# Optimization experiments

Hardware: AMD Instinct MI355X
Metric: run time of the kernel (lower is better)

The kernel has to match this reference:

```python
import jax, jax.numpy as jnp
import numpy as np

A = 16      # attention_beam_width
O = 8       # output_beam_width
H = 1024    # hidden_width
IO = 32     # io_width
DEPTH = 5   # GRU depth
T = 2048    # timesteps


def setup_inputs() -> dict:
    key = jax.random.key(0)
    ks = jax.random.split(key, 6)
    s = lambda k, shape: jax.random.normal(k, shape, dtype=jnp.float32) * 0.02
    return {
        "x": jax.random.normal(ks[0], (T, IO), dtype=jnp.float32),
        "w1": s(ks[1], (H, IO * A)),
        "b1": jnp.zeros((H,), jnp.float32),
        "gru_wih": s(ks[2], (DEPTH, 3 * H, H)),
        "gru_whh": s(ks[3], (DEPTH, 3 * H, H)),
        "gru_bih": jnp.zeros((DEPTH, 3 * H), jnp.float32),
        "gru_bhh": jnp.zeros((DEPTH, 3 * H), jnp.float32),
        "w2": s(ks[4], (IO * O, H)),
        "b2": jnp.zeros((IO * O,), jnp.float32),
    }


def _build_lines(x):
    # create_line at step t = concat([x[t], x[t-2], x[t-3], ..., x[t-A]])
    # (true_history[-i] for i=2..A before x[t] is appended; zeros for t-i < 0)
    Tn = x.shape[0]
    padded = jnp.concatenate([jnp.zeros((A, IO), x.dtype), x], axis=0)
    feats = [x] + [padded[A - i: A - i + Tn] for i in range(2, A + 1)]
    return jnp.concatenate(feats, axis=1)  # [T, IO*A]


def _gru_cell(h, xt, wih, whh, bih, bhh):
    # torch nn.GRU cell math (gate order r, z, n)
    gi = xt @ wih.T + bih      # [3H]
    gh = h @ whh.T + bhh       # [3H]
    i_r, i_z, i_n = jnp.split(gi, 3)
    h_r, h_z, h_n = jnp.split(gh, 3)
    r = jax.nn.sigmoid(i_r + h_r)
    z = jax.nn.sigmoid(i_z + h_z)
    n = jnp.tanh(i_n + r * h_n)
    return (1.0 - z) * n + z * h


def reference(x, w1, b1, gru_wih, gru_whh, gru_bih, gru_bhh, w2, b2):
    Tn = x.shape[0]
    lines = _build_lines(x)          # [T, IO*A]
    pre = lines @ w1.T + b1          # lin1, vectorized over time: [T, H]

    def step(h_all, xt):
        inp = xt
        new_h = []
        for l in range(DEPTH):  # fixed small depth loop
            h_new = _gru_cell(h_all[l], inp, gru_wih[l], gru_whh[l],
                              gru_bih[l], gru_bhh[l])
            new_h.append(h_new)
            inp = h_new
        return jnp.stack(new_h), inp

    h0 = jnp.zeros((DEPTH, H), x.dtype)
    _, gru_outs = jax.lax.scan(step, h0, pre)   # [T, H]
    out = gru_outs @ w2.T + b2                   # lin2: [T, IO*O]
    # per-step output is viewed (O, 1, IO) and cat along dim 1 -> [O, T, IO]
    return out.reshape(Tn, O, IO).transpose(1, 0, 2)
```

## Files before the change

kernel.cpp:

```cpp
#include <hip/hip_runtime.h>
#include <hip/hip_fp16.h>

typedef unsigned int u32;

#define TSTEPS 2048
#define HID    1024
#define NDEPTH 5
#define GSTAGE 51
#define NBLOCKS (NDEPTH * GSTAGE)
#define HCAN   0x7c00u
#define DCAN   0x7c007c00u

typedef _Float16 f16x2v __attribute__((ext_vector_type(2)));

#if defined(__has_builtin)
# if __has_builtin(__builtin_amdgcn_fdot2)
#  define HAVE_FDOT2 1
# endif
#endif

__device__ __forceinline__ float fdot2f(u32 a, u32 b, float c) {
  f16x2v x, y;
  __builtin_memcpy(&x, &a, 4);
  __builtin_memcpy(&y, &b, 4);
#ifdef HAVE_FDOT2
  return __builtin_amdgcn_fdot2(x, y, c, false);
#else
  return c + (float)x[0] * (float)y[0] + (float)x[1] * (float)y[1];
#endif
}

__device__ __forceinline__ u32 pkh(float a, float b) {
  __half2 h = __floats2half2_rn(a, b);
  u32 r;
  __builtin_memcpy(&r, &h, 4);
  return r;
}

__device__ __forceinline__ float dpp_red32(float v) {
  int t, vi;
  __builtin_memcpy(&vi, &v, 4);
  float tf;
#define STEP(CTRL)                                                        \
  t = __builtin_amdgcn_update_dpp(0, vi, CTRL, 0xF, 0xF, true);           \
  __builtin_memcpy(&tf, &t, 4);                                           \
  v += tf;                                                                \
  __builtin_memcpy(&vi, &v, 4);
  STEP(0x111)
  STEP(0x112)
  STEP(0x114)
  STEP(0x118)
  STEP(0x142)
#undef STEP
  return v;
}

__device__ __forceinline__ uint2 spin_load8(const void* p) {
  uint2 v;
  for (;;) {
    asm volatile("global_load_dwordx2 %0, %1, off sc0 sc1\n\ts_waitcnt vmcnt(0)"
                 : "=v"(v) : "v"(p));
    if (((v.x & 0xffffu) != HCAN) & ((v.x >> 16) != HCAN) &
        ((v.y & 0xffffu) != HCAN) & ((v.y >> 16) != HCAN))
      break;
    __builtin_amdgcn_s_sleep(1);
  }
  return v;
}

__global__ __launch_bounds__(256) void fill_canary(u32* __restrict__ p, long n) {
  long i = ((long)blockIdx.x * 256 + threadIdx.x) * 4;
  const long stride = (long)gridDim.x * 256 * 4;
  uint4 c;
  c.x = DCAN; c.y = DCAN; c.z = DCAN; c.w = DCAN;
  for (; i < n; i += stride) *(uint4*)(p + i) = c;
}

__global__ __launch_bounds__(256) void lin1_kernel(
    const float* __restrict__ x, const float* __restrict__ w1,
    const float* __restrict__ b1, __half* __restrict__ X0) {
  __shared__ float lt[32][65];
  __shared__ float wt[128][65];
  const int tid = threadIdx.x;
  const int t0 = blockIdx.x * 32;
  const int h0 = blockIdx.y * 128;
  const int tt0 = (tid & 7) * 4;
  const int hh0 = (tid >> 3) * 4;
  float acc[4][4] = {};
  for (int kc = 0; kc < 512; kc += 64) {
    __syncthreads();
#pragma unroll
    for (int m = 0; m < 8; ++m) {
      int e = tid + m * 256;
      int tt = e >> 6, kk = e & 63;
      int k = kc + kk;
      int a = k >> 5, io = k & 31;
      int d = (a == 0) ? 0 : (a + 1);
      int st = t0 + tt - d;
      lt[tt][kk] = (st >= 0) ? x[st * 32 + io] : 0.f;
    }
#pragma unroll
    for (int m = 0; m < 32; ++m) {
      int e = tid + m * 256;
      int hh = e >> 6, kk = e & 63;
      wt[hh][kk] = w1[(size_t)(h0 + hh) * 512 + kc + kk];
    }
    __syncthreads();
    for (int kk = 0; kk < 64; ++kk) {
      float la[4], wa[4];
#pragma unroll
      for (int i = 0; i < 4; ++i) la[i] = lt[tt0 + i][kk];
#pragma unroll
      for (int j = 0; j < 4; ++j) wa[j] = wt[hh0 + j][kk];
#pragma unroll
      for (int i = 0; i < 4; ++i)
#pragma unroll
        for (int j = 0; j < 4; ++j) acc[i][j] = fmaf(la[i], wa[j], acc[i][j]);
    }
  }
#pragma unroll
  for (int i = 0; i < 4; ++i)
#pragma unroll
    for (int j = 0; j < 4; ++j)
      X0[(size_t)(t0 + tt0 + i) * HID + h0 + hh0 + j] =
          __float2half_rn(acc[i][j] + b1[h0 + hh0 + j]);
}

__global__ __launch_bounds__(512, 2) void gru_pipe(
    const float* __restrict__ wih, const float* __restrict__ whh,
    const float* __restrict__ bih, const float* __restrict__ bhh,
    __half* __restrict__ Xh) {
  const int bid = blockIdx.x;
  const int l   = bid / GSTAGE;
  const int bs  = bid % GSTAGE;
  const int tid = (int)threadIdx.x;
  const int lane = tid & 63;
  const int wv   = tid >> 6;
  const int half = lane >> 5;
  const int kc   = lane & 31;
  const int RG   = 2 * wv + half;

  const int h_base = (bs * HID) / GSTAGE;
  const int h_cnt  = ((bs + 1) * HID) / GSTAGE - h_base;
  const int ndot = 3 * h_cnt;

  const size_t lw = (size_t)l * 3 * HID * HID;
  u32 wA[4][16], wB[4][16];
#pragma unroll
  for (int r = 0; r < 4; ++r) {
    const int d = 4 * RG + r;
    if (d < ndot) {
      const int jj = d / 3, g = d % 3;
      const float* rowA = wih + lw + (size_t)(g * HID + h_base + jj) * HID;
      const float* rowB = whh + lw + (size_t)(g * HID + h_base + jj) * HID;
#pragma unroll
      for (int s = 0; s < 4; ++s) {
        const float4* sa = (const float4*)(rowA + kc * 8 + s * 256);
        const float4* sb = (const float4*)(rowB + kc * 8 + s * 256);
        float4 a0 = sa[0], a1 = sa[1], b0 = sb[0], b1v = sb[1];
        wA[r][s * 4 + 0] = pkh(a0.x, a0.y);
        wA[r][s * 4 + 1] = pkh(a0.z, a0.w);
        wA[r][s * 4 + 2] = pkh(a1.x, a1.y);
        wA[r][s * 4 + 3] = pkh(a1.z, a1.w);
        wB[r][s * 4 + 0] = pkh(b0.x, b0.y);
        wB[r][s * 4 + 1] = pkh(b0.z, b0.w);
        wB[r][s * 4 + 2] = pkh(b1v.x, b1v.y);
        wB[r][s * 4 + 3] = pkh(b1v.z, b1v.w);
      }
    } else {
#pragma unroll
      for (int i = 0; i < 16; ++i) { wA[r][i] = 0u; wB[r][i] = 0u; }
    }
  }

  float b6[6] = {0.f, 0.f, 0.f, 0.f, 0.f, 0.f};
  if (wv == 0 && lane < h_cnt) {
#pragma unroll
    for (int g = 0; g < 3; ++g) {
      b6[g]     = bih[(size_t)l * 3 * HID + g * HID + h_base + lane];
      b6[3 + g] = bhh[(size_t)l * 3 * HID + g * HID + h_base + lane];
    }
  }

  __shared__ __align__(16) __half xbuf[2][HID];
  __shared__ __align__(16) __half hbuf[2][HID];
  __shared__ __align__(16) float scr[2][128];

  const __half* in = Xh + (size_t)l * TSTEPS * HID;
  __half* out      = Xh + (size_t)(l + 1) * TSTEPS * HID;

  if (wv >= 4) {
    const int i = tid - 256;
    uint2 v;
    if (l == 0) v = *(const uint2*)(in + 4 * i);
    else        v = spin_load8(in + 4 * i);
    ((uint2*)xbuf[0])[i] = v;
  }
  float hprev = 0.f;
  __syncthreads();

  for (int t = 0; t < TSTEPS; ++t) {
    const int p = t & 1;

    {
      const uint4* cp = (const uint4*)xbuf[p];
      float a0 = 0.f, a1 = 0.f, a2 = 0.f, a3 = 0.f;
#pragma unroll
      for (int s = 0; s < 4; ++s) {
        uint4 c = cp[kc + 32 * s];
        a0 = fdot2f(wA[0][4 * s + 0], c.x, a0);
        a1 = fdot2f(wA[1][4 * s + 0], c.x, a1);
        a2 = fdot2f(wA[2][4 * s + 0], c.x, a2);
        a3 = fdot2f(wA[3][4 * s + 0], c.x, a3);
        a0 = fdot2f(wA[0][4 * s + 1], c.y, a0);
        a1 = fdot2f(wA[1][4 * s + 1], c.y, a1);
        a2 = fdot2f(wA[2][4 * s + 1], c.y, a2);
        a3 = fdot2f(wA[3][4 * s + 1], c.y, a3);
        a0 = fdot2f(wA[0][4 * s + 2], c.z, a0);
        a1 = fdot2f(wA[1][4 * s + 2], c.z, a1);
        a2 = fdot2f(wA[2][4 * s + 2], c.z, a2);
        a3 = fdot2f(wA[3][4 * s + 2], c.z, a3);
        a0 = fdot2f(wA[0][4 * s + 3], c.w, a0);
        a1 = fdot2f(wA[1][4 * s + 3], c.w, a1);
        a2 = fdot2f(wA[2][4 * s + 3], c.w, a2);
        a3 = fdot2f(wA[3][4 * s + 3], c.w, a3);
      }
      a0 = dpp_red32(a0);
      a1 = dpp_red32(a1);
      a2 = dpp_red32(a2);
      a3 = dpp_red32(a3);
      if ((lane & 31) == 31) {
        float4 s4; s4.x = a0; s4.y = a1; s4.z = a2; s4.w = a3;
        *((float4*)&scr[p][4 * RG]) = s4;
      }
    }

    if (wv < 4) {
      if (t > 0) {
        uint2 v = spin_load8(out + (size_t)(t - 1) * HID + 4 * tid);
        ((uint2*)hbuf[p])[tid] = v;
      } else {
        uint2 z; z.x = 0u; z.y = 0u;
        ((uint2*)hbuf[p])[tid] = z;
      }
    } else {
      const int i = tid - 256;
      const int tn = (t + 1 < TSTEPS) ? (t + 1) : (TSTEPS - 1);
      uint2 v;
      if (l == 0) v = *(const uint2*)(in + (size_t)tn * HID + 4 * i);
      else        v = spin_load8(in + (size_t)tn * HID + 4 * i);
      ((uint2*)xbuf[p ^ 1])[i] = v;
    }
    __syncthreads();

    {
      const uint4* cp = (const uint4*)hbuf[p];
      float a0 = 0.f, a1 = 0.f, a2 = 0.f, a3 = 0.f;
#pragma unroll
      for (int s = 0; s < 4; ++s) {
        uint4 c = cp[kc + 32 * s];
        a0 = fdot2f(wB[0][4 * s + 0], c.x, a0);
        a1 = fdot2f(wB[1][4 * s + 0], c.x, a1);
        a2 = fdot2f(wB[2][4 * s + 0], c.x, a2);
        a3 = fdot2f(wB[3][4 * s + 0], c.x, a3);
        a0 = fdot2f(wB[0][4 * s + 1], c.y, a0);
        a1 = fdot2f(wB[1][4 * s + 1], c.y, a1);
        a2 = fdot2f(wB[2][4 * s + 1], c.y, a2);
        a3 = fdot2f(wB[3][4 * s + 1], c.y, a3);
        a0 = fdot2f(wB[0][4 * s + 2], c.z, a0);
        a1 = fdot2f(wB[1][4 * s + 2], c.z, a1);
        a2 = fdot2f(wB[2][4 * s + 2], c.z, a2);
        a3 = fdot2f(wB[3][4 * s + 2], c.z, a3);
        a0 = fdot2f(wB[0][4 * s + 3], c.w, a0);
        a1 = fdot2f(wB[1][4 * s + 3], c.w, a1);
        a2 = fdot2f(wB[2][4 * s + 3], c.w, a2);
        a3 = fdot2f(wB[3][4 * s + 3], c.w, a3);
      }
      a0 = dpp_red32(a0);
      a1 = dpp_red32(a1);
      a2 = dpp_red32(a2);
      a3 = dpp_red32(a3);
      if ((lane & 31) == 31) {
        float4 s4; s4.x = a0; s4.y = a1; s4.z = a2; s4.w = a3;
        *((float4*)&scr[p][64 + 4 * RG]) = s4;
      }
    }
    __syncthreads();

    if (wv == 0 && lane < h_cnt) {
      const int jj = lane;
      float ir = scr[p][3 * jj + 0] + b6[0];
      float iz = scr[p][3 * jj + 1] + b6[1];
      float in_ = scr[p][3 * jj + 2] + b6[2];
      float hr = scr[p][64 + 3 * jj + 0] + b6[3];
      float hz = scr[p][64 + 3 * jj + 1] + b6[4];
      float hn = scr[p][64 + 3 * jj + 2] + b6[5];
      float rr = 1.f / (1.f + __expf(-(ir + hr)));
      float zz = 1.f / (1.f + __expf(-(iz + hz)));
      float targ = in_ + rr * hn;
      targ = fminf(fmaxf(targ, -15.f), 15.f);
      float e2 = __expf(2.f * targ);
      float nn = (e2 - 1.f) / (e2 + 1.f);
      float hv = (1.f - zz) * nn + zz * hprev;
      hprev = hv;
      u32 hb = (u32)__half_as_ushort(__float2half_rn(hv));
      const __half* dst = out + (size_t)t * HID + h_base + jj;
      asm volatile("global_store_short %0, %1, off sc0 sc1" :: "v"(dst), "v"(hb));
    }
  }
}

__global__ __launch_bounds__(256) void lin2_kernel(
    const __half* __restrict__ h5, const float* __restrict__ w2,
    const float* __restrict__ b2, float* __restrict__ out) {
  __shared__ float at[64][65];
  __shared__ float bt[64][65];
  const int tid = threadIdx.x;
  const int t0 = blockIdx.x * 64;
  const int j0 = blockIdx.y * 64;
  const int tt0 = (tid & 15) * 4;
  const int jj0 = (tid >> 4) * 4;
  float acc[4][4] = {};
  for (int kc = 0; kc < 1024; kc += 64) {
    __syncthreads();
#pragma unroll
    for (int m = 0; m < 16; ++m) {
      int e = tid + m * 256;
      int tt = e >> 6, kk = e & 63;
      at[tt][kk] = __half2float(h5[(size_t)(t0 + tt) * HID + kc + kk]);
    }
#pragma unroll
    for (int m = 0; m < 16; ++m) {
      int e = tid + m * 256;
      int jj = e >> 6, kk = e & 63;
      bt[jj][kk] = w2[(size_t)(j0 + jj) * HID + kc + kk];
    }
    __syncthreads();
    for (int kk = 0; kk < 64; ++kk) {
      float la[4], wa[4];
#pragma unroll
      for (int i = 0; i < 4; ++i) la[i] = at[tt0 + i][kk];
#pragma unroll
      for (int j = 0; j < 4; ++j) wa[j] = bt[jj0 + j][kk];
#pragma unroll
      for (int i = 0; i < 4; ++i)
#pragma unroll
        for (int j = 0; j < 4; ++j) acc[i][j] = fmaf(la[i], wa[j], acc[i][j]);
    }
  }
#pragma unroll
  for (int i = 0; i < 4; ++i)
#pragma unroll
    for (int jq = 0; jq < 4; ++jq) {
      int j = j0 + jj0 + jq;
      out[(size_t)(j >> 5) * (TSTEPS * 32) + (size_t)(t0 + tt0 + i) * 32 + (j & 31)] =
          acc[i][jq] + b2[j];
    }
}

extern "C" void kernel_launch(void* const* d_in, const int* in_sizes, int n_in,
                              void* d_out, int out_size, void* d_ws, size_t ws_size,
                              hipStream_t stream) {
  const float* x   = (const float*)d_in[0];
  const float* w1  = (const float*)d_in[1];
  const float* b1  = (const float*)d_in[2];
  const float* wih = (const float*)d_in[3];
  const float* whh = (const float*)d_in[4];
  const float* bih = (const float*)d_in[5];
  const float* bhh = (const float*)d_in[6];
  const float* w2  = (const float*)d_in[7];
  const float* b2  = (const float*)d_in[8];
  float* out = (float*)d_out;

  __half* Xh = (__half*)d_ws;

  fill_canary<<<1280, 256, 0, stream>>>((u32*)(Xh + (size_t)TSTEPS * HID),
                                        (long)NDEPTH * TSTEPS * HID / 2);
  lin1_kernel<<<dim3(64, 8), 256, 0, stream>>>(x, w1, b1, Xh);
  gru_pipe<<<NBLOCKS, 512, 0, stream>>>(wih, whh, bih, bhh, Xh);
  lin2_kernel<<<dim3(32, 4), 256, 0, stream>>>(Xh + (size_t)NDEPTH * TSTEPS * HID,
                                               w2, b2, out);
}
```

Before: 3.517 ms.

## Load recurrent hidden state directly into registers, dropping LDS staging and a barrier

Each thread now polls the previous timestep's hidden-state slice it needs for the Whh dot products straight from global memory into registers, using four dwordx4 loads. This replaces the shared hbuf staging and removes one __syncthreads per timestep. The next-step x prefetch moves after the recurrent dot product, so it overlaps with the single remaining barrier. The canary check becomes a branch-free SWAR zero-halfword test, and the spin loop sleeps only after a few failed tries. In exchange, every wave issues redundant global polls of the same h row, which raises memory and L2 traffic.

```diff
diff --git a/kernel.cpp b/kernel.cpp
--- a/kernel.cpp
+++ b/kernel.cpp
@@ -35,6 +35,11 @@
   u32 r;
   __builtin_memcpy(&r, &h, 4);
   return r;
+}
+
+__device__ __forceinline__ u32 canz(u32 v) {
+  u32 t = v ^ DCAN;
+  return ((t - 0x00010001u) & ~t) & 0x80008000u;
 }
 
 __device__ __forceinline__ float dpp_red32(float v) {
@@ -57,15 +62,39 @@
 
 __device__ __forceinline__ uint2 spin_load8(const void* p) {
   uint2 v;
+  int tries = 0;
   for (;;) {
     asm volatile("global_load_dwordx2 %0, %1, off sc0 sc1\n\ts_waitcnt vmcnt(0)"
                  : "=v"(v) : "v"(p));
-    if (((v.x & 0xffffu) != HCAN) & ((v.x >> 16) != HCAN) &
-        ((v.y & 0xffffu) != HCAN) & ((v.y >> 16) != HCAN))
-      break;
-    __builtin_amdgcn_s_sleep(1);
+    if (!(canz(v.x) | canz(v.y))) break;
+    if (++tries > 2) __builtin_amdgcn_s_sleep(1);
   }
   return v;
+}
+
+__device__ __forceinline__ void spin_h4(const void* row, int kc, uint4 hc[4]) {
+  const uint4* p = (const uint4*)row + kc;
+  int tries = 0;
+  for (;;) {
+    uint4 a0, a1, a2, a3;
+    asm volatile(
+        "global_load_dwordx4 %0, %4, off sc0 sc1\n\t"
+        "global_load_dwordx4 %1, %5, off sc0 sc1\n\t"
+        "global_load_dwordx4 %2, %6, off sc0 sc1\n\t"
+        "global_load_dwordx4 %3, %7, off sc0 sc1\n\t"
+        "s_waitcnt vmcnt(0)"
+        : "=&v"(a0), "=&v"(a1), "=&v"(a2), "=&v"(a3)
+        : "v"(p), "v"(p + 32), "v"(p + 64), "v"(p + 96));
+    u32 bad = canz(a0.x) | canz(a0.y) | canz(a0.z) | canz(a0.w) |
+              canz(a1.x) | canz(a1.y) | canz(a1.z) | canz(a1.w) |
+              canz(a2.x) | canz(a2.y) | canz(a2.z) | canz(a2.w) |
+              canz(a3.x) | canz(a3.y) | canz(a3.z) | canz(a3.w);
+    if (!bad) {
+      hc[0] = a0; hc[1] = a1; hc[2] = a2; hc[3] = a3;
+      return;
+    }
+    if (++tries > 2) __builtin_amdgcn_s_sleep(1);
+  }
 }
 
 __global__ __launch_bounds__(256) void fill_canary(u32* __restrict__ p, long n) {
@@ -183,7 +212,6 @@
   }
 
   __shared__ __align__(16) __half xbuf[2][HID];
-  __shared__ __align__(16) __half hbuf[2][HID];
   __shared__ __align__(16) float scr[2][128];
 
   const __half* in = Xh + (size_t)l * TSTEPS * HID;
@@ -235,30 +263,19 @@
       }
     }
 
-    if (wv < 4) {
-      if (t > 0) {
-        uint2 v = spin_load8(out + (size_t)(t - 1) * HID + 4 * tid);
-        ((uint2*)hbuf[p])[tid] = v;
-      } else {
-        uint2 z; z.x = 0u; z.y = 0u;
-        ((uint2*)hbuf[p])[tid] = z;
-      }
+    uint4 hc[4];
+    if (t > 0) {
+      spin_h4(out + (size_t)(t - 1) * HID, kc, hc);
     } else {
-      const int i = tid - 256;
-      const int tn = (t + 1 < TSTEPS) ? (t + 1) : (TSTEPS - 1);
-      uint2 v;
-      if (l == 0) v = *(const uint2*)(in + (size_t)tn * HID + 4 * i);
-      else        v = spin_load8(in + (size_t)tn * HID + 4 * i);
-      ((uint2*)xbuf[p ^ 1])[i] = v;
-    }
-    __syncthreads();
+      uint4 z; z.x = 0u; z.y = 0u; z.z = 0u; z.w = 0u;
+      hc[0] = z; hc[1] = z; hc[2] = z; hc[3] = z;
+    }
 
     {
-      const uint4* cp = (const uint4*)hbuf[p];
       float a0 = 0.f, a1 = 0.f, a2 = 0.f, a3 = 0.f;
 #pragma unroll
       for (int s = 0; s < 4; ++s) {
-        uint4 c = cp[kc + 32 * s];
+        uint4 c = hc[s];
         a0 = fdot2f(wB[0][4 * s + 0], c.x, a0);
         a1 = fdot2f(wB[1][4 * s + 0], c.x, a1);
         a2 = fdot2f(wB[2][4 * s + 0], c.x, a2);
@@ -285,6 +302,16 @@
         *((float4*)&scr[p][64 + 4 * RG]) = s4;
       }
     }
+
+    if (wv >= 4) {
+      const int i = tid - 256;
+      const int tn = (t + 1 < TSTEPS) ? (t + 1) : (TSTEPS - 1);
+      uint2 v;
+      if (l == 0) v = *(const uint2*)(in + (size_t)tn * HID + 4 * i);
+      else        v = spin_load8(in + (size_t)tn * HID + 4 * i);
+      ((uint2*)xbuf[p ^ 1])[i] = v;
+    }
+
     __syncthreads();
 
     if (wv == 0 && lane < h_cnt) {
```

After: 5.604 ms. 1.59x slower.

## Give each hidden unit its own half-wave and drop the extra barrier in the GRU loop

Applied to the files above, without the earlier changes.

The GRU pipeline block is restructured so that each 32-lane half-wave owns one hidden unit and holds all three gate rows of both weight matrices. Each half-wave then computes the gate nonlinearity directly after its DPP reduction, which removes the shared scratch buffer and one __syncthreads per timestep. The block grows to 704 threads (22 half-waves for up to 21 units), and the input is prefetched two steps ahead through a triple buffer. The spin-wait canary check is vectorised and no longer sleeps on the first retries. The costs are a larger block, lanes that sit idle when they own no unit, and more polling traffic.

```diff
diff --git a/kernel.cpp b/kernel.cpp
--- a/kernel.cpp
+++ b/kernel.cpp
@@ -10,6 +10,7 @@
 #define NBLOCKS (NDEPTH * GSTAGE)
 #define HCAN   0x7c00u
 #define DCAN   0x7c007c00u
+#define THS    ((size_t)TSTEPS * HID)
 
 typedef _Float16 f16x2v __attribute__((ext_vector_type(2)));
 
@@ -35,6 +36,11 @@
   u32 r;
   __builtin_memcpy(&r, &h, 4);
   return r;
+}
+
+__device__ __forceinline__ u32 canz(u32 v) {
+  u32 t = v ^ DCAN;
+  return ((t - 0x00010001u) & ~t) & 0x80008000u;
 }
 
 __device__ __forceinline__ float dpp_red32(float v) {
@@ -57,13 +63,12 @@
 
 __device__ __forceinline__ uint2 spin_load8(const void* p) {
   uint2 v;
+  int tries = 0;
   for (;;) {
     asm volatile("global_load_dwordx2 %0, %1, off sc0 sc1\n\ts_waitcnt vmcnt(0)"
                  : "=v"(v) : "v"(p));
-    if (((v.x & 0xffffu) != HCAN) & ((v.x >> 16) != HCAN) &
-        ((v.y & 0xffffu) != HCAN) & ((v.y >> 16) != HCAN))
-      break;
-    __builtin_amdgcn_s_sleep(1);
+    if (!(canz(v.x) | canz(v.y))) break;
+    if (++tries > 2) __builtin_amdgcn_s_sleep(1);
   }
   return v;
 }
@@ -94,8 +99,8 @@
       int e = tid + m * 256;
       int tt = e >> 6, kk = e & 63;
       int k = kc + kk;
-      int a = k >> 5, io = k & 31;
-      int d = (a == 0) ? 0 : (a + 1);
+      int aa = k >> 5, io = k & 31;
+      int d = (aa == 0) ? 0 : (aa + 1);
       int st = t0 + tt - d;
       lt[tt][kk] = (st >= 0) ? x[st * 32 + io] : 0.f;
     }
@@ -126,187 +131,168 @@
           __float2half_rn(acc[i][j] + b1[h0 + hh0 + j]);
 }
 
-__global__ __launch_bounds__(512, 2) void gru_pipe(
+__global__ __launch_bounds__(704, 3) void gru_pipe(
     const float* __restrict__ wih, const float* __restrict__ whh,
     const float* __restrict__ bih, const float* __restrict__ bhh,
     __half* __restrict__ Xh) {
   const int bid = blockIdx.x;
-  const int l   = bid / GSTAGE;
-  const int bs  = bid % GSTAGE;
+  const int l  = bid / GSTAGE, bs = bid % GSTAGE;
   const int tid = (int)threadIdx.x;
-  const int lane = tid & 63;
-  const int wv   = tid >> 6;
-  const int half = lane >> 5;
-  const int kc   = lane & 31;
-  const int RG   = 2 * wv + half;
-
+  const int wv  = tid >> 6;
+  const int slot = tid >> 5;
+  const int kc   = tid & 31;
   const int h_base = (bs * HID) / GSTAGE;
   const int h_cnt  = ((bs + 1) * HID) / GSTAGE - h_base;
-  const int ndot = 3 * h_cnt;
-
+  const bool active = slot < h_cnt;
+
+  const __half* xin = Xh + (size_t)l * THS;
+  __half* hout      = Xh + (size_t)(l + 1) * THS;
+
+  u32 wA[3][16], wB[3][16];
   const size_t lw = (size_t)l * 3 * HID * HID;
-  u32 wA[4][16], wB[4][16];
-#pragma unroll
-  for (int r = 0; r < 4; ++r) {
-    const int d = 4 * RG + r;
-    if (d < ndot) {
-      const int jj = d / 3, g = d % 3;
-      const float* rowA = wih + lw + (size_t)(g * HID + h_base + jj) * HID;
-      const float* rowB = whh + lw + (size_t)(g * HID + h_base + jj) * HID;
+#pragma unroll
+  for (int g = 0; g < 3; ++g) {
+    if (active) {
+      const float* rowA = wih + lw + (size_t)(g * HID + h_base + slot) * HID;
+      const float* rowB = whh + lw + (size_t)(g * HID + h_base + slot) * HID;
 #pragma unroll
       for (int s = 0; s < 4; ++s) {
-        const float4* sa = (const float4*)(rowA + kc * 8 + s * 256);
-        const float4* sb = (const float4*)(rowB + kc * 8 + s * 256);
-        float4 a0 = sa[0], a1 = sa[1], b0 = sb[0], b1v = sb[1];
-        wA[r][s * 4 + 0] = pkh(a0.x, a0.y);
-        wA[r][s * 4 + 1] = pkh(a0.z, a0.w);
-        wA[r][s * 4 + 2] = pkh(a1.x, a1.y);
-        wA[r][s * 4 + 3] = pkh(a1.z, a1.w);
-        wB[r][s * 4 + 0] = pkh(b0.x, b0.y);
-        wB[r][s * 4 + 1] = pkh(b0.z, b0.w);
-        wB[r][s * 4 + 2] = pkh(b1v.x, b1v.y);
-        wB[r][s * 4 + 3] = pkh(b1v.z, b1v.w);
+        const float4* pa = (const float4*)(rowA + kc * 8 + s * 256);
+        const float4* pb = (const float4*)(rowB + kc * 8 + s * 256);
+        float4 a0 = pa[0], a1 = pa[1], b0 = pb[0], b1v = pb[1];
+        wA[g][4 * s + 0] = pkh(a0.x, a0.y);
+        wA[g][4 * s + 1] = pkh(a0.z, a0.w);
+        wA[g][4 * s + 2] = pkh(a1.x, a1.y);
+        wA[g][4 * s + 3] = pkh(a1.z, a1.w);
+        wB[g][4 * s + 0] = pkh(b0.x, b0.y);
+        wB[g][4 * s + 1] = pkh(b0.z, b0.w);
+        wB[g][4 * s + 2] = pkh(b1v.x, b1v.y);
+        wB[g][4 * s + 3] = pkh(b1v.z, b1v.w);
       }
     } else {
 #pragma unroll
-      for (int i = 0; i < 16; ++i) { wA[r][i] = 0u; wB[r][i] = 0u; }
-    }
-  }
-
-  float b6[6] = {0.f, 0.f, 0.f, 0.f, 0.f, 0.f};
-  if (wv == 0 && lane < h_cnt) {
-#pragma unroll
-    for (int g = 0; g < 3; ++g) {
-      b6[g]     = bih[(size_t)l * 3 * HID + g * HID + h_base + lane];
-      b6[3 + g] = bhh[(size_t)l * 3 * HID + g * HID + h_base + lane];
-    }
-  }
-
-  __shared__ __align__(16) __half xbuf[2][HID];
+      for (int j = 0; j < 16; ++j) { wA[g][j] = 0u; wB[g][j] = 0u; }
+    }
+  }
+
+  float Br = 0.f, Bz = 0.f, bin_ = 0.f, bhn_ = 0.f;
+  if (kc == 31 && active) {
+    const float* bi = bih + (size_t)l * 3 * HID + h_base + slot;
+    const float* bh = bhh + (size_t)l * 3 * HID + h_base + slot;
+    Br   = bi[0] + bh[0];
+    Bz   = bi[HID] + bh[HID];
+    bin_ = bi[2 * HID];
+    bhn_ = bh[2 * HID];
+  }
+
+  __shared__ __align__(16) __half xbuf[3][HID];
   __shared__ __align__(16) __half hbuf[2][HID];
-  __shared__ __align__(16) float scr[2][128];
-
-  const __half* in = Xh + (size_t)l * TSTEPS * HID;
-  __half* out      = Xh + (size_t)(l + 1) * TSTEPS * HID;
-
-  if (wv >= 4) {
+
+  if (wv >= 4 && wv < 8) {
     const int i = tid - 256;
-    uint2 v;
-    if (l == 0) v = *(const uint2*)(in + 4 * i);
-    else        v = spin_load8(in + 4 * i);
-    ((uint2*)xbuf[0])[i] = v;
-  }
+    uint2 v0, v1;
+    if (l == 0) {
+      v0 = *(const uint2*)(xin + 4 * i);
+      v1 = *(const uint2*)(xin + HID + 4 * i);
+    } else {
+      v0 = spin_load8(xin + 4 * i);
+      v1 = spin_load8(xin + HID + 4 * i);
+    }
+    ((uint2*)xbuf[0])[i] = v0;
+    ((uint2*)xbuf[1])[i] = v1;
+  }
+  __syncthreads();
+
   float hprev = 0.f;
-  __syncthreads();
-
+  int pr = 0;
   for (int t = 0; t < TSTEPS; ++t) {
-    const int p = t & 1;
-
+    const int ph = t & 1;
+
+    float ar = 0.f, az = 0.f, an = 0.f;
     {
-      const uint4* cp = (const uint4*)xbuf[p];
-      float a0 = 0.f, a1 = 0.f, a2 = 0.f, a3 = 0.f;
+      const uint4* cp = (const uint4*)xbuf[pr];
 #pragma unroll
       for (int s = 0; s < 4; ++s) {
         uint4 c = cp[kc + 32 * s];
-        a0 = fdot2f(wA[0][4 * s + 0], c.x, a0);
-        a1 = fdot2f(wA[1][4 * s + 0], c.x, a1);
-        a2 = fdot2f(wA[2][4 * s + 0], c.x, a2);
-        a3 = fdot2f(wA[3][4 * s + 0], c.x, a3);
-        a0 = fdot2f(wA[0][4 * s + 1], c.y, a0);
-        a1 = fdot2f(wA[1][4 * s + 1], c.y, a1);
-        a2 = fdot2f(wA[2][4 * s + 1], c.y, a2);
-        a3 = fdot2f(wA[3][4 * s + 1], c.y, a3);
-        a0 = fdot2f(wA[0][4 * s + 2], c.z, a0);
-        a1 = fdot2f(wA[1][4 * s + 2], c.z, a1);
-        a2 = fdot2f(wA[2][4 * s + 2], c.z, a2);
-        a3 = fdot2f(wA[3][4 * s + 2], c.z, a3);
-        a0 = fdot2f(wA[0][4 * s + 3], c.w, a0);
-        a1 = fdot2f(wA[1][4 * s + 3], c.w, a1);
-        a2 = fdot2f(wA[2][4 * s + 3], c.w, a2);
-        a3 = fdot2f(wA[3][4 * s + 3], c.w, a3);
+        ar = fdot2f(wA[0][4 * s + 0], c.x, ar);
+        az = fdot2f(wA[1][4 * s + 0], c.x, az);
+        an = fdot2f(wA[2][4 * s + 0], c.x, an);
+        ar = fdot2f(wA[0][4 * s + 1], c.y, ar);
+        az = fdot2f(wA[1][4 * s + 1], c.y, az);
+        an = fdot2f(wA[2][4 * s + 1], c.y, an);
+        ar = fdot2f(wA[0][4 * s + 2], c.z, ar);
+        az = fdot2f(wA[1][4 * s + 2], c.z, az);
+        an = fdot2f(wA[2][4 * s + 2], c.z, an);
+        ar = fdot2f(wA[0][4 * s + 3], c.w, ar);
+        az = fdot2f(wA[1][4 * s + 3], c.w, az);
+        an = fdot2f(wA[2][4 * s + 3], c.w, an);
       }
-      a0 = dpp_red32(a0);
-      a1 = dpp_red32(a1);
-      a2 = dpp_red32(a2);
-      a3 = dpp_red32(a3);
-      if ((lane & 31) == 31) {
-        float4 s4; s4.x = a0; s4.y = a1; s4.z = a2; s4.w = a3;
-        *((float4*)&scr[p][4 * RG]) = s4;
+    }
+    ar = dpp_red32(ar);
+    az = dpp_red32(az);
+    an = dpp_red32(an);
+
+    if (wv < 4) {
+      uint2 v;
+      if (t > 0) {
+        v = spin_load8(hout + (size_t)(t - 1) * HID + 4 * tid);
+      } else {
+        v.x = 0u; v.y = 0u;
       }
-    }
-
-    if (wv < 4) {
-      if (t > 0) {
-        uint2 v = spin_load8(out + (size_t)(t - 1) * HID + 4 * tid);
-        ((uint2*)hbuf[p])[tid] = v;
-      } else {
-        uint2 z; z.x = 0u; z.y = 0u;
-        ((uint2*)hbuf[p])[tid] = z;
-      }
-    } else {
+      ((uint2*)hbuf[ph])[tid] = v;
+    } else if (wv < 8) {
       const int i = tid - 256;
-      const int tn = (t + 1 < TSTEPS) ? (t + 1) : (TSTEPS - 1);
+      int tn = t + 2;
+      if (tn > TSTEPS - 1) tn = TSTEPS - 1;
       uint2 v;
-      if (l == 0) v = *(const uint2*)(in + (size_t)tn * HID + 4 * i);
-      else        v = spin_load8(in + (size_t)tn * HID + 4 * i);
-      ((uint2*)xbuf[p ^ 1])[i] = v;
-    }
-    __syncthreads();
-
+      if (l == 0) v = *(const uint2*)(xin + (size_t)tn * HID + 4 * i);
+      else        v = spin_load8(xin + (size_t)tn * HID + 4 * i);
+      int pw = pr + 2;
+      if (pw >= 3) pw -= 3;
+      ((uint2*)xbuf[pw])[i] = v;
+    }
+    __syncthreads();
+
+    float br = 0.f, bz = 0.f, bn = 0.f;
     {
-      const uint4* cp = (const uint4*)hbuf[p];
-      float a0 = 0.f, a1 = 0.f, a2 = 0.f, a3 = 0.f;
+      const uint4* cp = (const uint4*)hbuf[ph];
 #pragma unroll
       for (int s = 0; s < 4; ++s) {
         uint4 c = cp[kc + 32 * s];
-        a0 = fdot2f(wB[0][4 * s + 0], c.x, a0);
-        a1 = fdot2f(wB[1][4 * s + 0], c.x, a1);
-        a2 = fdot2f(wB[2][4 * s + 0], c.x, a2);
-        a3 = fdot2f(wB[3][4 * s + 0], c.x, a3);
-        a0 = fdot2f(wB[0][4 * s + 1], c.y, a0);
-        a1 = fdot2f(wB[1][4 * s + 1], c.y, a1);
-        a2 = fdot2f(wB[2][4 * s + 1], c.y, a2);
-        a3 = fdot2f(wB[3][4 * s + 1], c.y, a3);
-        a0 = fdot2f(wB[0][4 * s + 2], c.z, a0);
-        a1 = fdot2f(wB[1][4 * s + 2], c.z, a1);
-        a2 = fdot2f(wB[2][4 * s + 2], c.z, a2);
-        a3 = fdot2f(wB[3][4 * s + 2], c.z, a3);
-        a0 = fdot2f(wB[0][4 * s + 3], c.w, a0);
-        a1 = fdot2f(wB[1][4 * s + 3], c.w, a1);
-        a2 = fdot2f(wB[2][4 * s + 3], c.w, a2);
-        a3 = fdot2f(wB[3][4 * s + 3], c.w, a3);
+        br = fdot2f(wB[0][4 * s + 0], c.x, br);
+        bz = fdot2f(wB[1][4 * s + 0], c.x, bz);
+        bn = fdot2f(wB[2][4 * s + 0], c.x, bn);
+        br = fdot2f(wB[0][4 * s + 1], c.y, br);
+        bz = fdot2f(wB[1][4 * s + 1], c.y, bz);
+        bn = fdot2f(wB[2][4 * s + 1], c.y, bn);
+        br = fdot2f(wB[0][4 * s + 2], c.z, br);
+        bz = fdot2f(wB[1][4 * s + 2], c.z, bz);
+        bn = fdot2f(wB[2][4 * s + 2], c.z, bn);
+        br = fdot2f(wB[0][4 * s + 3], c.w, br);
+        bz = fdot2f(wB[1][4 * s + 3], c.w, bz);
+        bn = fdot2f(wB[2][4 * s + 3], c.w, bn);
       }
-      a0 = dpp_red32(a0);
-      a1 = dpp_red32(a1);
-      a2 = dpp_red32(a2);
-      a3 = dpp_red32(a3);
-      if ((lane & 31) == 31) {
-        float4 s4; s4.x = a0; s4.y = a1; s4.z = a2; s4.w = a3;
-        *((float4*)&scr[p][64 + 4 * RG]) = s4;
-      }
-    }
-    __syncthreads();
-
-    if (wv == 0 && lane < h_cnt) {
-      const int jj = lane;
-      float ir = scr[p][3 * jj + 0] + b6[0];
-      float iz = scr[p][3 * jj + 1] + b6[1];
-      float in_ = scr[p][3 * jj + 2] + b6[2];
-      float hr = scr[p][64 + 3 * jj + 0] + b6[3];
-      float hz = scr[p][64 + 3 * jj + 1] + b6[4];
-      float hn = scr[p][64 + 3 * jj + 2] + b6[5];
-      float rr = 1.f / (1.f + __expf(-(ir + hr)));
-      float zz = 1.f / (1.f + __expf(-(iz + hz)));
-      float targ = in_ + rr * hn;
+    }
+    br = dpp_red32(br);
+    bz = dpp_red32(bz);
+    bn = dpp_red32(bn);
+
+    if (kc == 31 && active) {
+      float rr = 1.f / (1.f + __expf(-(ar + br + Br)));
+      float zz = 1.f / (1.f + __expf(-(az + bz + Bz)));
+      float targ = (an + bin_) + rr * (bn + bhn_);
       targ = fminf(fmaxf(targ, -15.f), 15.f);
       float e2 = __expf(2.f * targ);
       float nn = (e2 - 1.f) / (e2 + 1.f);
       float hv = (1.f - zz) * nn + zz * hprev;
       hprev = hv;
       u32 hb = (u32)__half_as_ushort(__float2half_rn(hv));
-      const __half* dst = out + (size_t)t * HID + h_base + jj;
+      const __half* dst = hout + (size_t)t * HID + h_base + slot;
       asm volatile("global_store_short %0, %1, off sc0 sc1" :: "v"(dst), "v"(hb));
     }
+
+    pr += 1;
+    if (pr >= 3) pr -= 3;
   }
 }
 
@@ -374,10 +360,10 @@
 
   __half* Xh = (__half*)d_ws;
 
-  fill_canary<<<1280, 256, 0, stream>>>((u32*)(Xh + (size_t)TSTEPS * HID),
-                                        (long)NDEPTH * TSTEPS * HID / 2);
+  fill_canary<<<1280, 256, 0, stream>>>((u32*)(Xh + THS),
+                                        (long)NDEPTH * (long)THS / 2);
   lin1_kernel<<<dim3(64, 8), 256, 0, stream>>>(x, w1, b1, Xh);
-  gru_pipe<<<NBLOCKS, 512, 0, stream>>>(wih, whh, bih, bhh, Xh);
-  lin2_kernel<<<dim3(32, 4), 256, 0, stream>>>(Xh + (size_t)NDEPTH * TSTEPS * HID,
+  gru_pipe<<<NBLOCKS, 704, 0, stream>>>(wih, whh, bih, bhh, Xh);
+  lin2_kernel<<<dim3(32, 4), 256, 0, stream>>>(Xh + (size_t)NDEPTH * THS,
                                                w2, b2, out);
 }
```

After: 7.303 ms. 108% more time.

## Triple-buffer input prefetch two steps ahead and spread gate math across waves

Applied to the files above, without the earlier changes.

The layer-input buffer grows from two to three slots so each step prefetches the input for t+2 instead of t+1. This relaxes the cross-layer dependency, so the spin-wait on the upstream layer less often stalls the step. The gate nonlinearity is split across four waves with six lanes each instead of one wave, and the spin loop uses a bitwise canary check and skips the sleep on its first few tries. The cost is more shared memory, more polling traffic, and a ring-index bookkeeping step each iteration.

```diff
diff --git a/kernel.cpp b/kernel.cpp
--- a/kernel.cpp
+++ b/kernel.cpp
@@ -10,6 +10,7 @@
 #define NBLOCKS (NDEPTH * GSTAGE)
 #define HCAN   0x7c00u
 #define DCAN   0x7c007c00u
+#define THS    ((size_t)TSTEPS * HID)
 
 typedef _Float16 f16x2v __attribute__((ext_vector_type(2)));
 
@@ -35,6 +36,11 @@
   u32 r;
   __builtin_memcpy(&r, &h, 4);
   return r;
+}
+
+__device__ __forceinline__ u32 canz(u32 v) {
+  u32 t = v ^ DCAN;
+  return ((t - 0x00010001u) & ~t) & 0x80008000u;
 }
 
 __device__ __forceinline__ float dpp_red32(float v) {
@@ -57,13 +63,12 @@
 
 __device__ __forceinline__ uint2 spin_load8(const void* p) {
   uint2 v;
+  int tries = 0;
   for (;;) {
     asm volatile("global_load_dwordx2 %0, %1, off sc0 sc1\n\ts_waitcnt vmcnt(0)"
                  : "=v"(v) : "v"(p));
-    if (((v.x & 0xffffu) != HCAN) & ((v.x >> 16) != HCAN) &
-        ((v.y & 0xffffu) != HCAN) & ((v.y >> 16) != HCAN))
-      break;
-    __builtin_amdgcn_s_sleep(1);
+    if (!(canz(v.x) | canz(v.y))) break;
+    if (++tries > 2) __builtin_amdgcn_s_sleep(1);
   }
   return v;
 }
@@ -94,8 +99,8 @@
       int e = tid + m * 256;
       int tt = e >> 6, kk = e & 63;
       int k = kc + kk;
-      int a = k >> 5, io = k & 31;
-      int d = (a == 0) ? 0 : (a + 1);
+      int aa = k >> 5, io = k & 31;
+      int d = (aa == 0) ? 0 : (aa + 1);
       int st = t0 + tt - d;
       lt[tt][kk] = (st >= 0) ? x[st * 32 + io] : 0.f;
     }
@@ -131,8 +136,7 @@
     const float* __restrict__ bih, const float* __restrict__ bhh,
     __half* __restrict__ Xh) {
   const int bid = blockIdx.x;
-  const int l   = bid / GSTAGE;
-  const int bs  = bid % GSTAGE;
+  const int l  = bid / GSTAGE, bs = bid % GSTAGE;
   const int tid = (int)threadIdx.x;
   const int lane = tid & 63;
   const int wv   = tid >> 6;
@@ -173,37 +177,46 @@
     }
   }
 
+  const int jjg = 6 * wv + lane;
+  const bool gate_owner = (wv < 4) && (lane < 6) && (jjg < h_cnt);
   float b6[6] = {0.f, 0.f, 0.f, 0.f, 0.f, 0.f};
-  if (wv == 0 && lane < h_cnt) {
+  if (gate_owner) {
 #pragma unroll
     for (int g = 0; g < 3; ++g) {
-      b6[g]     = bih[(size_t)l * 3 * HID + g * HID + h_base + lane];
-      b6[3 + g] = bhh[(size_t)l * 3 * HID + g * HID + h_base + lane];
-    }
-  }
-
-  __shared__ __align__(16) __half xbuf[2][HID];
+      b6[g]     = bih[(size_t)l * 3 * HID + g * HID + h_base + jjg];
+      b6[3 + g] = bhh[(size_t)l * 3 * HID + g * HID + h_base + jjg];
+    }
+  }
+
+  __shared__ __align__(16) __half xbuf[3][HID];
   __shared__ __align__(16) __half hbuf[2][HID];
   __shared__ __align__(16) float scr[2][128];
 
-  const __half* in = Xh + (size_t)l * TSTEPS * HID;
-  __half* out      = Xh + (size_t)(l + 1) * TSTEPS * HID;
+  const __half* in = Xh + (size_t)l * THS;
+  __half* out      = Xh + (size_t)(l + 1) * THS;
 
   if (wv >= 4) {
     const int i = tid - 256;
-    uint2 v;
-    if (l == 0) v = *(const uint2*)(in + 4 * i);
-    else        v = spin_load8(in + 4 * i);
-    ((uint2*)xbuf[0])[i] = v;
+    uint2 v0, v1;
+    if (l == 0) {
+      v0 = *(const uint2*)(in + 4 * i);
+      v1 = *(const uint2*)(in + HID + 4 * i);
+    } else {
+      v0 = spin_load8(in + 4 * i);
+      v1 = spin_load8(in + HID + 4 * i);
+    }
+    ((uint2*)xbuf[0])[i] = v0;
+    ((uint2*)xbuf[1])[i] = v1;
   }
   float hprev = 0.f;
   __syncthreads();
 
+  int rx = 0;
   for (int t = 0; t < TSTEPS; ++t) {
     const int p = t & 1;
 
     {
-      const uint4* cp = (const uint4*)xbuf[p];
+      const uint4* cp = (const uint4*)xbuf[rx];
       float a0 = 0.f, a1 = 0.f, a2 = 0.f, a3 = 0.f;
 #pragma unroll
       for (int s = 0; s < 4; ++s) {
@@ -236,20 +249,21 @@
     }
 
     if (wv < 4) {
+      uint2 v;
       if (t > 0) {
-        uint2 v = spin_load8(out + (size_t)(t - 1) * HID + 4 * tid);
-        ((uint2*)hbuf[p])[tid] = v;
+        v = spin_load8(out + (size_t)(t - 1) * HID + 4 * tid);
       } else {
-        uint2 z; z.x = 0u; z.y = 0u;
-        ((uint2*)hbuf[p])[tid] = z;
-      }
-    } else {
+        v.x = 0u; v.y = 0u;
+      }
+      ((uint2*)hbuf[p])[tid] = v;
+    } else if (t + 2 < TSTEPS) {
       const int i = tid - 256;
-      const int tn = (t + 1 < TSTEPS) ? (t + 1) : (TSTEPS - 1);
+      int pw = rx + 2;
+      if (pw >= 3) pw -= 3;
       uint2 v;
-      if (l == 0) v = *(const uint2*)(in + (size_t)tn * HID + 4 * i);
-      else        v = spin_load8(in + (size_t)tn * HID + 4 * i);
-      ((uint2*)xbuf[p ^ 1])[i] = v;
+      if (l == 0) v = *(const uint2*)(in + (size_t)(t + 2) * HID + 4 * i);
+      else        v = spin_load8(in + (size_t)(t + 2) * HID + 4 * i);
+      ((uint2*)xbuf[pw])[i] = v;
     }
     __syncthreads();
 
@@ -287,14 +301,13 @@
     }
     __syncthreads();
 
-    if (wv == 0 && lane < h_cnt) {
-      const int jj = lane;
-      float ir = scr[p][3 * jj + 0] + b6[0];
-      float iz = scr[p][3 * jj + 1] + b6[1];
-      float in_ = scr[p][3 * jj + 2] + b6[2];
-      float hr = scr[p][64 + 3 * jj + 0] + b6[3];
-      float hz = scr[p][64 + 3 * jj + 1] + b6[4];
-      float hn = scr[p][64 + 3 * jj + 2] + b6[5];
+    if (gate_owner) {
+      float ir = scr[p][3 * jjg + 0] + b6[0];
+      float iz = scr[p][3 * jjg + 1] + b6[1];
+      float in_ = scr[p][3 * jjg + 2] + b6[2];
+      float hr = scr[p][64 + 3 * jjg + 0] + b6[3];
+      float hz = scr[p][64 + 3 * jjg + 1] + b6[4];
+      float hn = scr[p][64 + 3 * jjg + 2] + b6[5];
       float rr = 1.f / (1.f + __expf(-(ir + hr)));
       float zz = 1.f / (1.f + __expf(-(iz + hz)));
       float targ = in_ + rr * hn;
@@ -304,9 +317,12 @@
       float hv = (1.f - zz) * nn + zz * hprev;
       hprev = hv;
       u32 hb = (u32)__half_as_ushort(__float2half_rn(hv));
-      const __half* dst = out + (size_t)t * HID + h_base + jj;
+      const __half* dst = out + (size_t)t * HID + h_base + jjg;
       asm volatile("global_store_short %0, %1, off sc0 sc1" :: "v"(dst), "v"(hb));
     }
+
+    rx += 1;
+    if (rx >= 3) rx -= 3;
   }
 }
 
@@ -374,10 +390,10 @@
 
   __half* Xh = (__half*)d_ws;
 
-  fill_canary<<<1280, 256, 0, stream>>>((u32*)(Xh + (size_t)TSTEPS * HID),
-                                        (long)NDEPTH * TSTEPS * HID / 2);
+  fill_canary<<<1280, 256, 0, stream>>>((u32*)(Xh + THS),
+                                        (long)NDEPTH * (long)THS / 2);
   lin1_kernel<<<dim3(64, 8), 256, 0, stream>>>(x, w1, b1, Xh);
   gru_pipe<<<NBLOCKS, 512, 0, stream>>>(wih, whh, bih, bhh, Xh);
-  lin2_kernel<<<dim3(32, 4), 256, 0, stream>>>(Xh + (size_t)NDEPTH * TSTEPS * HID,
+  lin2_kernel<<<dim3(32, 4), 256, 0, stream>>>(Xh + (size_t)NDEPTH * THS,
                                                w2, b2, out);
 }
```

New measurement: 3.293 ms. 1.07x faster.
